# Optimization experiments

Measured on AMD Instinct MI355X. Metric: run time of the kernel, lower is better.

Reference implementation:

```python
import jax, jax.numpy as jnp
import numpy as np

SMOOTH = 1.0
IGNORE_INDEX = 255


def setup_inputs() -> dict:
    key = jax.random.key(0)
    k1, k2 = jax.random.split(key)
    B, C, H, W = 8, 19, 512, 512
    logits = jax.random.normal(k1, (B, C, H, W), dtype=jnp.float32)
    targets = jax.random.randint(k2, (B, H, W), 0, C, dtype=jnp.int64)
    return {"logits": logits, "targets": targets}


def reference(logits, targets):
    B, C, H, W = logits.shape
    probs = jax.nn.softmax(logits, axis=1)                      # [B,C,H,W]
    valid = targets != IGNORE_INDEX                             # [B,H,W] bool
    vf = valid.astype(probs.dtype)                              # [B,H,W]
    # clamp invalid labels to 0; their contributions are zeroed by vf
    t = jnp.where(valid, targets, 0).reshape(-1)                # [B*H*W]
    # per-class sum of probs over valid pixels (replaces boolean compaction)
    probs_sum = jnp.einsum('bchw,bhw->c', probs, vf)            # [C]
    # prob assigned to the true class at each pixel (replaces one-hot * probs)
    gathered = jnp.take_along_axis(probs, jnp.where(valid, targets, 0)[:, None], axis=1)[:, 0]  # [B,H,W]
    gathered = (gathered * vf).reshape(-1)
    intersection = jnp.zeros((C,), probs.dtype).at[t].add(gathered)   # [C]
    counts = jnp.zeros((C,), probs.dtype).at[t].add(vf.reshape(-1))   # [C] = one_hot.sum(0)
    union = probs_sum + counts
    dice = (2.0 * intersection + SMOOTH) / (union + SMOOTH)
    loss = (1.0 - dice).mean()
    # torch returns logits.sum()*0 when no valid pixels
    return jnp.where(vf.sum() > 0, loss, logits.sum() * 0.0)
```

## Files before the change

kernel.cpp:

```cpp
#include <hip/hip_runtime.h>
#include <hip/hip_bf16.h>
#include <math.h>


#define CC 19
#define HWBITS 18
#define HHWW (1 << HWBITS)
#define NPIX (8 * HHWW)
#define NBLK 1024
#define NTHR 256
#define IGNORE_IDX 255

__global__ __launch_bounds__(NTHR, 2) void dice_accum(
    const float* __restrict__ logits,
    const int* __restrict__ targets,
    float* __restrict__ part)
{
    const int tid = blockIdx.x * NTHR + threadIdx.x;
    const int stride = NBLK * NTHR;

    float accS[CC], accI[CC];
#pragma unroll
    for (int c = 0; c < CC; ++c) { accS[c] = 0.f; accI[c] = 0.f; }
    int cnt[CC];
#pragma unroll
    for (int c = 0; c < CC; ++c) cnt[c] = 0;

    for (int p = tid; p < NPIX; p += stride) {
        const int t = targets[p];
        const int b = p >> HWBITS;
        const int hw = p & (HHWW - 1);
        const float* base = logits + ((size_t)(b * CC) << HWBITS) + hw;

        float e[CC];
        float s = 0.f;
#pragma unroll
        for (int c = 0; c < CC; ++c) {
            e[c] = __expf(base[(size_t)c << HWBITS]);
            s += e[c];
        }
        const bool valid = (t != IGNORE_IDX);
        const float inv = valid ? __builtin_amdgcn_rcpf(s) : 0.f;

#pragma unroll
        for (int c = 0; c < CC; ++c) {
            accS[c] = fmaf(e[c], inv, accS[c]);
            const bool hit = (t == c);
            accI[c] = fmaf(hit ? e[c] : 0.f, inv, accI[c]);
            cnt[c] += (int)__popcll(__ballot(hit));
        }
    }

#pragma unroll
    for (int c = 0; c < CC; ++c) {
        for (int off = 32; off; off >>= 1) {
            accS[c] += __shfl_down(accS[c], off);
            accI[c] += __shfl_down(accI[c], off);
        }
    }

    __shared__ float s_part[4][64];
    const int wave = threadIdx.x >> 6;
    const int lane = threadIdx.x & 63;
    if (lane == 0) {
#pragma unroll
        for (int c = 0; c < CC; ++c) {
            s_part[wave][c]          = accS[c];
            s_part[wave][CC + c]     = accI[c];
            s_part[wave][2 * CC + c] = (float)cnt[c];
        }
#pragma unroll
        for (int c = 3 * CC; c < 64; ++c) s_part[wave][c] = 0.f;
    }
    __syncthreads();
    if (threadIdx.x < 64) {
        float v = s_part[0][threadIdx.x] + s_part[1][threadIdx.x]
                + s_part[2][threadIdx.x] + s_part[3][threadIdx.x];
        part[blockIdx.x * 64 + threadIdx.x] = v;
    }
}

__global__ __launch_bounds__(1024) void dice_final(
    const float* __restrict__ part, float* __restrict__ out)
{
    const int wave = threadIdx.x >> 6;
    const int lane = threadIdx.x & 63;
    float v = 0.f;
    for (int r = wave; r < NBLK; r += 16)
        v += part[r * 64 + lane];

    __shared__ float s_red[16][64];
    s_red[wave][lane] = v;
    __syncthreads();

    __shared__ float s_tot[64];
    if (threadIdx.x < 64) {
        float tot = 0.f;
#pragma unroll
        for (int w = 0; w < 16; ++w) tot += s_red[w][threadIdx.x];
        s_tot[threadIdx.x] = tot;
    }
    __syncthreads();

    if (threadIdx.x == 0) {
        float loss = 0.f, totv = 0.f;
#pragma unroll
        for (int c = 0; c < CC; ++c) {
            const float S = s_tot[c];
            const float I = s_tot[CC + c];
            const float N = s_tot[2 * CC + c];
            totv += N;
            loss += 1.f - (2.f * I + 1.f) / (S + N + 1.f);
        }
        out[0] = (totv > 0.f) ? loss * (1.f / (float)CC) : 0.f;
    }
}

extern "C" void kernel_launch(void* const* d_in, const int* in_sizes, int n_in,
                              void* d_out, int out_size, void* d_ws, size_t ws_size,
                              hipStream_t stream) {
    const float* logits = (const float*)d_in[0];
    const int* targets = (const int*)d_in[1];
    float* part = (float*)d_ws;
    float* out = (float*)d_out;

    dice_accum<<<NBLK, NTHR, 0, stream>>>(logits, targets, part);
    dice_final<<<1, 1024, 0, stream>>>(part, out);
}
```

Before: 246.7 us.

## Stage logit tiles in LDS with float4 loads and LDS-atomic class bins

Each block now loads 512-pixel tiles of all 19 channels into shared memory with float4 loads, then each thread handles two pixels, recomputing exp in a second pass instead of holding them in registers. Per-class intersection and counts are accumulated with shared-memory atomics on the true class rather than per-class predicated FMAs and ballots. This aims for wider coalesced global reads and fewer per-pixel ops. In exchange it adds 38KB of LDS per block, which limits occupancy, plus an extra sync per tile, recomputed exponentials, and atomic contention on 38 bins.

```diff
diff --git a/kernel.cpp b/kernel.cpp
--- a/kernel.cpp
+++ b/kernel.cpp
@@ -7,76 +7,97 @@
 #define HWBITS 18
 #define HHWW (1 << HWBITS)
 #define NPIX (8 * HHWW)
+#define TP 512
+#define TILEF4 (CC * TP / 4)
 #define NBLK 1024
 #define NTHR 256
+#define TILES_PER_BLK 4
 #define IGNORE_IDX 255
 
-__global__ __launch_bounds__(NTHR, 2) void dice_accum(
+__global__ __launch_bounds__(NTHR) void dice_accum(
     const float* __restrict__ logits,
     const int* __restrict__ targets,
     float* __restrict__ part)
 {
-    const int tid = blockIdx.x * NTHR + threadIdx.x;
-    const int stride = NBLK * NTHR;
+    __shared__ float xs[CC * TP];
+    __shared__ float s_bins[2 * CC];
+    __shared__ float s_part[4][64];
 
-    float accS[CC], accI[CC];
+    const int tid = threadIdx.x;
+    if (tid < 2 * CC) s_bins[tid] = 0.f;
+
+    float accS[CC];
 #pragma unroll
-    for (int c = 0; c < CC; ++c) { accS[c] = 0.f; accI[c] = 0.f; }
-    int cnt[CC];
-#pragma unroll
-    for (int c = 0; c < CC; ++c) cnt[c] = 0;
+    for (int c = 0; c < CC; ++c) accS[c] = 0.f;
 
-    for (int p = tid; p < NPIX; p += stride) {
-        const int t = targets[p];
-        const int b = p >> HWBITS;
-        const int hw = p & (HHWW - 1);
-        const float* base = logits + ((size_t)(b * CC) << HWBITS) + hw;
+    for (int it = 0; it < TILES_PER_BLK; ++it) {
+        const int tile = blockIdx.x * TILES_PER_BLK + it;
+        const int p0 = tile * TP;
+        const int b = p0 >> HWBITS;
+        const int hw0 = p0 & (HHWW - 1);
+        const float* bb = logits + ((size_t)(b * CC) << HWBITS) + hw0;
 
-        float e[CC];
-        float s = 0.f;
+        __syncthreads();
+        for (int j = tid; j < TILEF4; j += NTHR) {
+            const int c = j >> 7;
+            const int o4 = j & 127;
+            const float4 v = *(const float4*)(bb + ((size_t)c << HWBITS) + o4 * 4);
+            *(float4*)&xs[j * 4] = v;
+        }
+        const int2 tt = *(const int2*)(targets + p0 + 2 * tid);
+        __syncthreads();
+
+        float s0 = 0.f, s1 = 0.f;
 #pragma unroll
         for (int c = 0; c < CC; ++c) {
-            e[c] = __expf(base[(size_t)c << HWBITS]);
-            s += e[c];
+            const float2 v = *(const float2*)&xs[c * TP + 2 * tid];
+            s0 += __expf(v.x);
+            s1 += __expf(v.y);
         }
-        const bool valid = (t != IGNORE_IDX);
-        const float inv = valid ? __builtin_amdgcn_rcpf(s) : 0.f;
+        const bool v0 = (tt.x != IGNORE_IDX);
+        const bool v1 = (tt.y != IGNORE_IDX);
+        const float inv0 = v0 ? __builtin_amdgcn_rcpf(s0) : 0.f;
+        const float inv1 = v1 ? __builtin_amdgcn_rcpf(s1) : 0.f;
 
 #pragma unroll
         for (int c = 0; c < CC; ++c) {
-            accS[c] = fmaf(e[c], inv, accS[c]);
-            const bool hit = (t == c);
-            accI[c] = fmaf(hit ? e[c] : 0.f, inv, accI[c]);
-            cnt[c] += (int)__popcll(__ballot(hit));
+            const float2 v = *(const float2*)&xs[c * TP + 2 * tid];
+            accS[c] = fmaf(__expf(v.x), inv0, accS[c]);
+            accS[c] = fmaf(__expf(v.y), inv1, accS[c]);
+        }
+
+        if (v0) {
+            const float pt = __expf(xs[tt.x * TP + 2 * tid]) * inv0;
+            atomicAdd(&s_bins[tt.x], pt);
+            atomicAdd(&s_bins[CC + tt.x], 1.f);
+        }
+        if (v1) {
+            const float pt = __expf(xs[tt.y * TP + 2 * tid + 1]) * inv1;
+            atomicAdd(&s_bins[tt.y], pt);
+            atomicAdd(&s_bins[CC + tt.y], 1.f);
         }
     }
 
 #pragma unroll
     for (int c = 0; c < CC; ++c) {
-        for (int off = 32; off; off >>= 1) {
+        for (int off = 32; off; off >>= 1)
             accS[c] += __shfl_down(accS[c], off);
-            accI[c] += __shfl_down(accI[c], off);
-        }
     }
-
-    __shared__ float s_part[4][64];
-    const int wave = threadIdx.x >> 6;
-    const int lane = threadIdx.x & 63;
+    const int wave = tid >> 6;
+    const int lane = tid & 63;
     if (lane == 0) {
 #pragma unroll
-        for (int c = 0; c < CC; ++c) {
-            s_part[wave][c]          = accS[c];
-            s_part[wave][CC + c]     = accI[c];
-            s_part[wave][2 * CC + c] = (float)cnt[c];
-        }
+        for (int c = 0; c < CC; ++c) s_part[wave][c] = accS[c];
 #pragma unroll
-        for (int c = 3 * CC; c < 64; ++c) s_part[wave][c] = 0.f;
+        for (int c = CC; c < 64; ++c) s_part[wave][c] = 0.f;
     }
     __syncthreads();
-    if (threadIdx.x < 64) {
-        float v = s_part[0][threadIdx.x] + s_part[1][threadIdx.x]
-                + s_part[2][threadIdx.x] + s_part[3][threadIdx.x];
-        part[blockIdx.x * 64 + threadIdx.x] = v;
+    if (tid < 64) {
+        float v = s_part[0][tid] + s_part[1][tid]
+                + s_part[2][tid] + s_part[3][tid];
+        if (tid >= CC && tid < 3 * CC)
+            v += s_bins[tid - CC];
+        part[blockIdx.x * 64 + tid] = v;
     }
 }
 
```

New measurement: 255.0 us. 3.4% more time.

## Stage logit tiles into LDS via global_load_lds and process four pixels per thread

Applied to the files above, without the earlier changes.

Replaces the grid-stride per-pixel loop with one 1024-pixel tile per block, loaded directly into shared memory with 16-byte global_load_lds DMA for all 19 channels and the targets. Each thread then computes exp, softmax normalization and the per-class sums for four pixels using vector LDS accesses, and replaces the ballot/popcount counting with per-lane float counts reduced by shuffles. The aim is wider, more efficient memory transactions and less per-pixel instruction overhead. The ~80KB LDS footprint limits occupancy, there is no overlap between loading and compute within a block, and the block count doubles the partial buffer size.

```diff
diff --git a/kernel.cpp b/kernel.cpp
--- a/kernel.cpp
+++ b/kernel.cpp
@@ -7,48 +7,77 @@
 #define HWBITS 18
 #define HHWW (1 << HWBITS)
 #define NPIX (8 * HHWW)
-#define NBLK 1024
+#define TP 1024
+#define NBLK (NPIX / TP)
 #define NTHR 256
 #define IGNORE_IDX 255
 
-__global__ __launch_bounds__(NTHR, 2) void dice_accum(
+typedef const __attribute__((address_space(1))) void g_void_t;
+typedef __attribute__((address_space(3))) void lds_void_t;
+
+__device__ __forceinline__ void dma16(const void* g, void* l) {
+    __builtin_amdgcn_global_load_lds((g_void_t*)g, (lds_void_t*)l, 16, 0, 0);
+}
+
+__global__ __launch_bounds__(NTHR) void dice_accum(
     const float* __restrict__ logits,
     const int* __restrict__ targets,
     float* __restrict__ part)
 {
-    const int tid = blockIdx.x * NTHR + threadIdx.x;
-    const int stride = NBLK * NTHR;
+    __shared__ float xs[CC * TP];
+    __shared__ int   ts[TP];
 
-    float accS[CC], accI[CC];
+    const int tid = threadIdx.x;
+    const int wave = tid >> 6;
+    const int lane = tid & 63;
+
+    const int p0 = blockIdx.x * TP;
+    const int b = p0 >> HWBITS;
+    const int hw0 = p0 & (HHWW - 1);
+
+    for (int c = wave; c < CC; c += 4) {
+        const float* g = logits + (((size_t)(b * CC + c)) << HWBITS) + hw0 + lane * 4;
+        float* l = &xs[c * TP];
 #pragma unroll
-    for (int c = 0; c < CC; ++c) { accS[c] = 0.f; accI[c] = 0.f; }
-    int cnt[CC];
+        for (int k = 0; k < 4; ++k)
+            dma16(g + k * 256, l + k * 256);
+    }
+    if (wave == 3) {
+        const int* g = targets + p0 + lane * 4;
 #pragma unroll
-    for (int c = 0; c < CC; ++c) cnt[c] = 0;
+        for (int k = 0; k < 4; ++k)
+            dma16(g + k * 256, &ts[k * 256]);
+    }
+    __syncthreads();
 
-    for (int p = tid; p < NPIX; p += stride) {
-        const int t = targets[p];
-        const int b = p >> HWBITS;
-        const int hw = p & (HHWW - 1);
-        const float* base = logits + ((size_t)(b * CC) << HWBITS) + hw;
+    const int4 tt = *(const int4*)&ts[4 * tid];
+    float4 s4 = make_float4(0.f, 0.f, 0.f, 0.f);
+#pragma unroll
+    for (int c = 0; c < CC; ++c) {
+        float4 v = *(float4*)&xs[c * TP + 4 * tid];
+        v.x = __expf(v.x); v.y = __expf(v.y);
+        v.z = __expf(v.z); v.w = __expf(v.w);
+        *(float4*)&xs[c * TP + 4 * tid] = v;
+        s4.x += v.x; s4.y += v.y; s4.z += v.z; s4.w += v.w;
+    }
+    const float i0 = (tt.x != IGNORE_IDX) ? __builtin_amdgcn_rcpf(s4.x) : 0.f;
+    const float i1 = (tt.y != IGNORE_IDX) ? __builtin_amdgcn_rcpf(s4.y) : 0.f;
+    const float i2 = (tt.z != IGNORE_IDX) ? __builtin_amdgcn_rcpf(s4.z) : 0.f;
+    const float i3 = (tt.w != IGNORE_IDX) ? __builtin_amdgcn_rcpf(s4.w) : 0.f;
 
-        float e[CC];
-        float s = 0.f;
+    float accS[CC], accI[CC], accC[CC];
 #pragma unroll
-        for (int c = 0; c < CC; ++c) {
-            e[c] = __expf(base[(size_t)c << HWBITS]);
-            s += e[c];
-        }
-        const bool valid = (t != IGNORE_IDX);
-        const float inv = valid ? __builtin_amdgcn_rcpf(s) : 0.f;
-
-#pragma unroll
-        for (int c = 0; c < CC; ++c) {
-            accS[c] = fmaf(e[c], inv, accS[c]);
-            const bool hit = (t == c);
-            accI[c] = fmaf(hit ? e[c] : 0.f, inv, accI[c]);
-            cnt[c] += (int)__popcll(__ballot(hit));
-        }
+    for (int c = 0; c < CC; ++c) {
+        const float4 e = *(const float4*)&xs[c * TP + 4 * tid];
+        accS[c] = fmaf(e.x, i0, fmaf(e.y, i1, fmaf(e.z, i2, e.w * i3)));
+        const bool h0 = (tt.x == c), h1 = (tt.y == c);
+        const bool h2 = (tt.z == c), h3 = (tt.w == c);
+        accI[c] = fmaf(h0 ? e.x : 0.f, i0,
+                  fmaf(h1 ? e.y : 0.f, i1,
+                  fmaf(h2 ? e.z : 0.f, i2,
+                       (h3 ? e.w : 0.f) * i3)));
+        accC[c] = (h0 ? 1.f : 0.f) + (h1 ? 1.f : 0.f)
+                + (h2 ? 1.f : 0.f) + (h3 ? 1.f : 0.f);
     }
 
 #pragma unroll
@@ -56,27 +85,26 @@
         for (int off = 32; off; off >>= 1) {
             accS[c] += __shfl_down(accS[c], off);
             accI[c] += __shfl_down(accI[c], off);
+            accC[c] += __shfl_down(accC[c], off);
         }
     }
-
-    __shared__ float s_part[4][64];
-    const int wave = threadIdx.x >> 6;
-    const int lane = threadIdx.x & 63;
+    __syncthreads();
+    float* s_part = xs;
     if (lane == 0) {
 #pragma unroll
         for (int c = 0; c < CC; ++c) {
-            s_part[wave][c]          = accS[c];
-            s_part[wave][CC + c]     = accI[c];
-            s_part[wave][2 * CC + c] = (float)cnt[c];
+            s_part[wave * 64 + c]          = accS[c];
+            s_part[wave * 64 + CC + c]     = accI[c];
+            s_part[wave * 64 + 2 * CC + c] = accC[c];
         }
 #pragma unroll
-        for (int c = 3 * CC; c < 64; ++c) s_part[wave][c] = 0.f;
+        for (int c = 3 * CC; c < 64; ++c) s_part[wave * 64 + c] = 0.f;
     }
     __syncthreads();
-    if (threadIdx.x < 64) {
-        float v = s_part[0][threadIdx.x] + s_part[1][threadIdx.x]
-                + s_part[2][threadIdx.x] + s_part[3][threadIdx.x];
-        part[blockIdx.x * 64 + threadIdx.x] = v;
+    if (tid < 64) {
+        const float v = s_part[tid] + s_part[64 + tid]
+                      + s_part[128 + tid] + s_part[192 + tid];
+        part[blockIdx.x * 64 + tid] = v;
     }
 }
 
```

New measurement: 258.0 us. +4.6%, slower.

## Vectorize pixel loads to float4 and double-buffer a fixed unrolled iteration schedule

Applied to the files above, without the earlier changes.

Each thread now processes four adjacent pixels per step using 128-bit nontemporal loads for logits and targets, instead of one pixel per scalar load. The grid-stride loop becomes four fully unrolled quads with two register buffers, so the loads for the next quad are issued while the current one is computed. Wave-ballot counting is replaced by per-thread float counters reduced with shuffles, and the block count is halved. The change adds heavy register pressure (two 19-element float4 buffers plus 57 accumulators), which may lower occupancy or cause spills. It also hardcodes the iteration count to the exact input size.

```diff
diff --git a/kernel.cpp b/kernel.cpp
--- a/kernel.cpp
+++ b/kernel.cpp
@@ -7,9 +7,57 @@
 #define HWBITS 18
 #define HHWW (1 << HWBITS)
 #define NPIX (8 * HHWW)
-#define NBLK 1024
+#define QPP (HHWW / 4)
+#define NQUAD (NPIX / 4)
+#define NBLK 512
 #define NTHR 256
+#define NTH_TOT (NBLK * NTHR)
+#define NITER (NQUAD / NTH_TOT)
 #define IGNORE_IDX 255
+
+typedef float f32x4 __attribute__((ext_vector_type(4)));
+typedef int   i32x4 __attribute__((ext_vector_type(4)));
+
+#define LOADQ(X, T, IT) do {                                                  \
+    const int q_ = tid + (IT) * NTH_TOT;                                      \
+    const int b_ = q_ >> 16;                                                  \
+    const int hw4_ = q_ & (QPP - 1);                                          \
+    const f32x4* base_ = (const f32x4*)logits + (size_t)(b_ * CC) * QPP + hw4_; \
+    _Pragma("unroll")                                                         \
+    for (int c = 0; c < CC; ++c)                                              \
+        X[c] = __builtin_nontemporal_load(base_ + (size_t)c * QPP);           \
+    T = __builtin_nontemporal_load((const i32x4*)(targets + 4 * (size_t)q_)); \
+} while (0)
+
+#define COMPUTE(X, T) do {                                                    \
+    float s0 = 0.f, s1 = 0.f, s2 = 0.f, s3 = 0.f;                             \
+    _Pragma("unroll")                                                         \
+    for (int c = 0; c < CC; ++c) {                                            \
+        X[c].x = __expf(X[c].x); s0 += X[c].x;                                \
+        X[c].y = __expf(X[c].y); s1 += X[c].y;                                \
+        X[c].z = __expf(X[c].z); s2 += X[c].z;                                \
+        X[c].w = __expf(X[c].w); s3 += X[c].w;                                \
+    }                                                                         \
+    const float i0 = (T.x != IGNORE_IDX) ? __builtin_amdgcn_rcpf(s0) : 0.f;   \
+    const float i1 = (T.y != IGNORE_IDX) ? __builtin_amdgcn_rcpf(s1) : 0.f;   \
+    const float i2 = (T.z != IGNORE_IDX) ? __builtin_amdgcn_rcpf(s2) : 0.f;   \
+    const float i3 = (T.w != IGNORE_IDX) ? __builtin_amdgcn_rcpf(s3) : 0.f;   \
+    _Pragma("unroll")                                                         \
+    for (int c = 0; c < CC; ++c) {                                            \
+        accS[c] = fmaf(X[c].x, i0,                                            \
+                  fmaf(X[c].y, i1,                                            \
+                  fmaf(X[c].z, i2,                                            \
+                  fmaf(X[c].w, i3, accS[c]))));                               \
+        const bool h0 = (T.x == c), h1 = (T.y == c);                          \
+        const bool h2 = (T.z == c), h3 = (T.w == c);                          \
+        accI[c] = fmaf(h0 ? X[c].x : 0.f, i0,                                 \
+                  fmaf(h1 ? X[c].y : 0.f, i1,                                 \
+                  fmaf(h2 ? X[c].z : 0.f, i2,                                 \
+                  fmaf(h3 ? X[c].w : 0.f, i3, accI[c]))));                    \
+        accC[c] += (h0 ? 1.f : 0.f) + (h1 ? 1.f : 0.f)                        \
+                 + (h2 ? 1.f : 0.f) + (h3 ? 1.f : 0.f);                       \
+    }                                                                         \
+} while (0)
 
 __global__ __launch_bounds__(NTHR, 2) void dice_accum(
     const float* __restrict__ logits,
@@ -17,45 +65,29 @@
     float* __restrict__ part)
 {
     const int tid = blockIdx.x * NTHR + threadIdx.x;
-    const int stride = NBLK * NTHR;
 
-    float accS[CC], accI[CC];
+    float accS[CC], accI[CC], accC[CC];
 #pragma unroll
-    for (int c = 0; c < CC; ++c) { accS[c] = 0.f; accI[c] = 0.f; }
-    int cnt[CC];
-#pragma unroll
-    for (int c = 0; c < CC; ++c) cnt[c] = 0;
+    for (int c = 0; c < CC; ++c) { accS[c] = 0.f; accI[c] = 0.f; accC[c] = 0.f; }
 
-    for (int p = tid; p < NPIX; p += stride) {
-        const int t = targets[p];
-        const int b = p >> HWBITS;
-        const int hw = p & (HHWW - 1);
-        const float* base = logits + ((size_t)(b * CC) << HWBITS) + hw;
+    f32x4 xa[CC], xb[CC];
+    i32x4 ta, tb;
 
-        float e[CC];
-        float s = 0.f;
-#pragma unroll
-        for (int c = 0; c < CC; ++c) {
-            e[c] = __expf(base[(size_t)c << HWBITS]);
-            s += e[c];
-        }
-        const bool valid = (t != IGNORE_IDX);
-        const float inv = valid ? __builtin_amdgcn_rcpf(s) : 0.f;
-
-#pragma unroll
-        for (int c = 0; c < CC; ++c) {
-            accS[c] = fmaf(e[c], inv, accS[c]);
-            const bool hit = (t == c);
-            accI[c] = fmaf(hit ? e[c] : 0.f, inv, accI[c]);
-            cnt[c] += (int)__popcll(__ballot(hit));
-        }
-    }
+    LOADQ(xa, ta, 0);
+    LOADQ(xb, tb, 1);
+    COMPUTE(xa, ta);
+    LOADQ(xa, ta, 2);
+    COMPUTE(xb, tb);
+    LOADQ(xb, tb, 3);
+    COMPUTE(xa, ta);
+    COMPUTE(xb, tb);
 
 #pragma unroll
     for (int c = 0; c < CC; ++c) {
         for (int off = 32; off; off >>= 1) {
             accS[c] += __shfl_down(accS[c], off);
             accI[c] += __shfl_down(accI[c], off);
+            accC[c] += __shfl_down(accC[c], off);
         }
     }
 
@@ -67,7 +99,7 @@
         for (int c = 0; c < CC; ++c) {
             s_part[wave][c]          = accS[c];
             s_part[wave][CC + c]     = accI[c];
-            s_part[wave][2 * CC + c] = (float)cnt[c];
+            s_part[wave][2 * CC + c] = accC[c];
         }
 #pragma unroll
         for (int c = 3 * CC; c < 64; ++c) s_part[wave][c] = 0.f;
```

Result: no change. 242.7 us (-1.6%).
